# Kernel tuning notes

Measured on AMD Instinct MI355X. Metric: run time of the kernel, lower is better.

## Reference

```python
import jax, jax.numpy as jnp
import numpy as np

BS, H, S, D = 2, 16, 4096, 64
BLOCK = 64
STRIDE_C = 3
NEG = -10000.0


def _global_index(seq_len, block_size, stride_c):
    # static Longformer-style global pattern: first token of each block plus
    # the last `stride_c` tokens of each block
    r = np.arange(seq_len)
    rem = r % block_size
    return np.nonzero((rem == 0) | (rem >= block_size - stride_c))[0]


def setup_inputs() -> dict:
    key = jax.random.key(0)
    k1, k2, k3 = jax.random.split(key, 3)
    q = jax.random.normal(k1, (BS, H, S, D), dtype=jnp.float32)
    k = jax.random.normal(k2, (BS, H, S, D), dtype=jnp.float32)
    v = jax.random.normal(k3, (BS, H, S, D), dtype=jnp.float32)
    mask = jnp.ones((BS, S), dtype=jnp.float32)  # all tokens valid -> pattern is static
    return {"query": q, "key": k, "value": v, "mask": mask}


def reference(query, key, value, mask):
    bs, h, S, d = query.shape
    block = BLOCK
    nb = S // block  # seq_len chosen as multiple of block_size, so pad_len == 0
    g_idx = jnp.asarray(_global_index(S, block, STRIDE_C))  # [G]

    # ---- block-local attention scores ----
    bq = query.reshape(bs, h, nb, block, d)
    bk = key.reshape(bs, h, nb, block, d)
    local = jnp.einsum('bhnxd,bhnyd->bhnxy', bq, bk)  # [bs,h,nb,block,block]
    # additive key-side mask (per key position within each block)
    key_mask = jnp.where(mask == 0.0, NEG, 0.0).reshape(bs, 1, nb, 1, block)
    local = (local + key_mask).reshape(bs, h, S, block)

    # ---- global-token attention scores ----
    gk = key[:, :, g_idx, :]    # [bs,h,G,d]
    gv = value[:, :, g_idx, :]  # [bs,h,G,d]
    gscores = jnp.einsum('bhsd,bhgd->bhsg', query, gk)  # [bs,h,S,G]
    gmask = jnp.where(mask[:, g_idx] == 0.0, NEG, 0.0)[:, None, None, :]
    gscores = gscores + gmask

    # ---- joint softmax over [local block | global tokens] ----
    scores = jnp.concatenate([local, gscores], axis=-1)  # [bs,h,S,block+G]
    probs = jax.nn.softmax(scores.astype(jnp.float32), axis=-1)

    # ---- weighted sums ----
    lp = probs[..., :block].reshape(bs, h, nb, block, block)
    bv = value.reshape(bs, h, nb, block, d)
    lout = jnp.matmul(lp, bv).reshape(bs, h, S, d)
    gout = jnp.einsum('bhsg,bhgd->bhsd', probs[..., block:], gv)
    return lout + gout
```

## Files before the change

### kernel.cpp

```cpp
#include <hip/hip_runtime.h>
#include <math.h>

#define BSZ 2
#define NH 16
#define SEQ 4096
#define DH 64
#define BLK 64
#define NB (SEQ / BLK)
#define NG 256
#define NKEY (BLK + NG)
#define NEGV -10000.0f
#define KSTR 72
#define PSTR2 168

typedef _Float16 f16x8 __attribute__((ext_vector_type(8)));
typedef _Float16 f16x4 __attribute__((ext_vector_type(4)));
typedef float floatx4 __attribute__((ext_vector_type(4)));

__device__ __forceinline__ int gather_row(int g) {
    int j = g >> 2;
    int p = g & 3;
    return j * BLK + (p ? (BLK - 4 + p) : 0);
}

__global__ __launch_bounds__(256, 2)
void sparse_attn_kernel(const float* __restrict__ Q, const float* __restrict__ K,
                        const float* __restrict__ V, const float* __restrict__ M,
                        float* __restrict__ O)
{
    const int wg   = blockIdx.x;
    const int nblk = wg & (NB - 1);
    const int bh   = wg >> 6;
    const int b    = bh >> 4;

    const size_t hoff = (size_t)bh * SEQ * DH;
    const float* Qh = Q + hoff;
    const float* Kh = K + hoff;
    const float* Vh = V + hoff;
    float*       Oh = O + hoff;
    const float* Mb = M + (size_t)b * SEQ;

    __shared__ _Float16 Ksh[NKEY * KSTR];
    __shared__ float    MaskAdd[NKEY];
    _Float16* Psh = Ksh;
    _Float16* VTc = Ksh + 64 * PSTR2;

    const int tid  = threadIdx.x;
    const int lane = tid & 63;
    const int wv   = tid >> 6;
    const int m    = lane & 15;
    const int quad = lane >> 4;

    for (int i = tid; i < NKEY * 16; i += 256) {
        int row = i >> 4;
        int c4  = (i & 15) << 2;
        int srow = (row < BLK) ? (nblk * BLK + row) : gather_row(row - BLK);
        const float4 f = *(const float4*)(Kh + (size_t)srow * DH + c4);
        f16x4 o4;
        o4[0] = (_Float16)f.x; o4[1] = (_Float16)f.y;
        o4[2] = (_Float16)f.z; o4[3] = (_Float16)f.w;
        *(f16x4*)(&Ksh[row * KSTR + c4]) = o4;
    }
    for (int i = tid; i < NKEY; i += 256) {
        int srow = (i < BLK) ? (nblk * BLK + i) : gather_row(i - BLK);
        MaskAdd[i] = (Mb[srow] == 0.0f) ? NEGV : 0.0f;
    }

    const int qrow = nblk * BLK + wv * 16 + m;
    f16x8 qhf[2], qlf[2];
    #pragma unroll
    for (int c = 0; c < 2; ++c) {
        const float* src = Qh + (size_t)qrow * DH + c * 32 + quad * 8;
        float4 f0 = *(const float4*)(src);
        float4 f1 = *(const float4*)(src + 4);
        float vals[8] = {f0.x, f0.y, f0.z, f0.w, f1.x, f1.y, f1.z, f1.w};
        #pragma unroll
        for (int j = 0; j < 8; ++j) {
            _Float16 hi = (_Float16)vals[j];
            float    lo = vals[j] - (float)hi;
            qhf[c][j] = hi;
            qlf[c][j] = (_Float16)lo;
        }
    }

    __syncthreads();

    floatx4 acc[20] = {};
    #pragma unroll
    for (int t = 0; t < 20; ++t) {
        #pragma unroll
        for (int c = 0; c < 2; ++c) {
            f16x8 kf = *(const f16x8*)(&Ksh[(t * 16 + m) * KSTR + c * 32 + quad * 8]);
            acc[t] = __builtin_amdgcn_mfma_f32_16x16x32_f16(qhf[c], kf, acc[t], 0, 0, 0);
            acc[t] = __builtin_amdgcn_mfma_f32_16x16x32_f16(qlf[c], kf, acc[t], 0, 0, 0);
        }
    }

    float rmax[4] = {-3e38f, -3e38f, -3e38f, -3e38f};
    #pragma unroll
    for (int t = 0; t < 20; ++t) {
        float ma = MaskAdd[t * 16 + m];
        #pragma unroll
        for (int r = 0; r < 4; ++r) {
            acc[t][r] += ma;
            rmax[r] = fmaxf(rmax[r], acc[t][r]);
        }
    }
    #pragma unroll
    for (int off = 8; off >= 1; off >>= 1) {
        #pragma unroll
        for (int r = 0; r < 4; ++r)
            rmax[r] = fmaxf(rmax[r], __shfl_xor(rmax[r], off, 64));
    }
    float rsum[4] = {0.f, 0.f, 0.f, 0.f};
    #pragma unroll
    for (int t = 0; t < 20; ++t) {
        #pragma unroll
        for (int r = 0; r < 4; ++r) {
            float e = __expf(acc[t][r] - rmax[r]);
            acc[t][r] = e;
            rsum[r] += e;
        }
    }
    #pragma unroll
    for (int off = 8; off >= 1; off >>= 1) {
        #pragma unroll
        for (int r = 0; r < 4; ++r)
            rsum[r] += __shfl_xor(rsum[r], off, 64);
    }
    float rinv[4];
    #pragma unroll
    for (int r = 0; r < 4; ++r) rinv[r] = 1.0f / rsum[r];

    __syncthreads();

    floatx4 oacc[4] = {};
    for (int cch = 0; cch < 2; ++cch) {
        #pragma unroll
        for (int t = 0; t < 10; ++t) {
            int tt = cch * 10 + t;
            #pragma unroll
            for (int r = 0; r < 4; ++r)
                Psh[(wv * 16 + quad * 4 + r) * PSTR2 + t * 16 + m] =
                    (_Float16)(acc[tt][r] * rinv[r]);
        }
        for (int i = tid; i < 160 * 16; i += 256) {
            int key = (i >> 4) + cch * 160;
            int c4  = (i & 15) << 2;
            int srow = (key < BLK) ? (nblk * BLK + key) : gather_row(key - BLK);
            const float4 f = *(const float4*)(Vh + (size_t)srow * DH + c4);
            int kl = key - cch * 160;
            VTc[(c4 + 0) * PSTR2 + kl] = (_Float16)f.x;
            VTc[(c4 + 1) * PSTR2 + kl] = (_Float16)f.y;
            VTc[(c4 + 2) * PSTR2 + kl] = (_Float16)f.z;
            VTc[(c4 + 3) * PSTR2 + kl] = (_Float16)f.w;
        }
        __syncthreads();
        #pragma unroll
        for (int kc = 0; kc < 5; ++kc) {
            f16x8 pf = *(const f16x8*)(&Psh[(wv * 16 + m) * PSTR2 + kc * 32 + quad * 8]);
            #pragma unroll
            for (int t = 0; t < 4; ++t) {
                f16x8 vf = *(const f16x8*)(&VTc[(t * 16 + m) * PSTR2 + kc * 32 + quad * 8]);
                oacc[t] = __builtin_amdgcn_mfma_f32_16x16x32_f16(pf, vf, oacc[t], 0, 0, 0);
            }
        }
        __syncthreads();
    }

    #pragma unroll
    for (int t = 0; t < 4; ++t) {
        #pragma unroll
        for (int r = 0; r < 4; ++r)
            Oh[(size_t)(nblk * BLK + wv * 16 + quad * 4 + r) * DH + t * 16 + m] = oacc[t][r];
    }
}

extern "C" void kernel_launch(void* const* d_in, const int* in_sizes, int n_in,
                              void* d_out, int out_size, void* d_ws, size_t ws_size,
                              hipStream_t stream) {
    const float* q    = (const float*)d_in[0];
    const float* k    = (const float*)d_in[1];
    const float* v    = (const float*)d_in[2];
    const float* mask = (const float*)d_in[3];
    float* out = (float*)d_out;
    (void)in_sizes; (void)n_in; (void)out_size; (void)d_ws; (void)ws_size;
    sparse_attn_kernel<<<BSZ * NH * NB, 256, 0, stream>>>(q, k, v, mask, out);
}
```

Measured before the change: 181.3 us.

## Rewrite sparse attention kernel with MFMA-native smem layouts and prefetched V

Drops the hi/lo split of Q, so the QK^T MFMA count is halved and precision is lower. K, P and V^T are now stored in shared memory in fragment-contiguous slabs so each lane reads one f16x8 at lane*8. V loads are issued early into registers so they overlap the QK and softmax phases. The mask is folded into the accumulator init and normalization is deferred to the output store. The change also remaps the block index to interleave heads, cuts LDS to raise occupancy to 4 workgroups per CU, and accepts higher register pressure from the prefetched V.

```diff
diff --git a/kernel.cpp b/kernel.cpp
--- a/kernel.cpp
+++ b/kernel.cpp
@@ -1,179 +1,232 @@
 #include <hip/hip_runtime.h>
-#include <math.h>
-
-#define BSZ 2
-#define NH 16
-#define SEQ 4096
-#define DH 64
-#define BLK 64
-#define NB (SEQ / BLK)
-#define NG 256
-#define NKEY (BLK + NG)
+
 #define NEGV -10000.0f
-#define KSTR 72
-#define PSTR2 168
 
 typedef _Float16 f16x8 __attribute__((ext_vector_type(8)));
-typedef _Float16 f16x4 __attribute__((ext_vector_type(4)));
+typedef _Float16 f16x2 __attribute__((ext_vector_type(2)));
 typedef float floatx4 __attribute__((ext_vector_type(4)));
 
-__device__ __forceinline__ int gather_row(int g) {
-    int j = g >> 2;
+__device__ __forceinline__ int src_row(int key, int nblk) {
+    if (key < 64) return nblk * 64 + key;
+    int g = key - 64;
     int p = g & 3;
-    return j * BLK + (p ? (BLK - 4 + p) : 0);
+    return (g >> 2) * 64 + (p ? (60 + p) : 0);
 }
 
-__global__ __launch_bounds__(256, 2)
+__global__ __launch_bounds__(256, 4)
 void sparse_attn_kernel(const float* __restrict__ Q, const float* __restrict__ K,
                         const float* __restrict__ V, const float* __restrict__ M,
                         float* __restrict__ O)
 {
-    const int wg   = blockIdx.x;
-    const int nblk = wg & (NB - 1);
-    const int bh   = wg >> 6;
+    const int x    = blockIdx.x;
+    const int bh   = (x & 7) * 4 + ((x >> 3) >> 6);
+    const int nblk = (x >> 3) & 63;
     const int b    = bh >> 4;
 
-    const size_t hoff = (size_t)bh * SEQ * DH;
+    const size_t hoff = (size_t)bh * (4096 * 64);
     const float* Qh = Q + hoff;
     const float* Kh = K + hoff;
     const float* Vh = V + hoff;
     float*       Oh = O + hoff;
-    const float* Mb = M + (size_t)b * SEQ;
-
-    __shared__ _Float16 Ksh[NKEY * KSTR];
-    __shared__ float    MaskAdd[NKEY];
-    _Float16* Psh = Ksh;
-    _Float16* VTc = Ksh + 64 * PSTR2;
+    const float* Mb = M + (size_t)b * 4096;
+
+    __shared__ _Float16 smem[20480];
+    _Float16* Pbase  = smem;
+    _Float16* VTbase = smem + 10240;
 
     const int tid  = threadIdx.x;
     const int lane = tid & 63;
     const int wv   = tid >> 6;
     const int m    = lane & 15;
     const int quad = lane >> 4;
-
-    for (int i = tid; i < NKEY * 16; i += 256) {
-        int row = i >> 4;
-        int c4  = (i & 15) << 2;
-        int srow = (row < BLK) ? (nblk * BLK + row) : gather_row(row - BLK);
-        const float4 f = *(const float4*)(Kh + (size_t)srow * DH + c4);
-        f16x4 o4;
-        o4[0] = (_Float16)f.x; o4[1] = (_Float16)f.y;
-        o4[2] = (_Float16)f.z; o4[3] = (_Float16)f.w;
-        *(f16x4*)(&Ksh[row * KSTR + c4]) = o4;
-    }
-    for (int i = tid; i < NKEY; i += 256) {
-        int srow = (i < BLK) ? (nblk * BLK + i) : gather_row(i - BLK);
-        MaskAdd[i] = (Mb[srow] == 0.0f) ? NEGV : 0.0f;
-    }
-
-    const int qrow = nblk * BLK + wv * 16 + m;
-    f16x8 qhf[2], qlf[2];
+    const int cg   = tid & 15;
+    const int psub = tid >> 4;
+
+    float mreg[20];
+    #pragma unroll
+    for (int t = 0; t < 20; ++t) {
+        int key = t * 16 + m;
+        mreg[t] = (Mb[src_row(key, nblk)] == 0.0f) ? NEGV : 0.0f;
+    }
+
+    const int qrow = nblk * 64 + wv * 16 + m;
+    f16x8 qf[2];
     #pragma unroll
     for (int c = 0; c < 2; ++c) {
-        const float* src = Qh + (size_t)qrow * DH + c * 32 + quad * 8;
-        float4 f0 = *(const float4*)(src);
+        const float* src = Qh + (size_t)qrow * 64 + c * 32 + quad * 8;
+        float4 f0 = *(const float4*)src;
         float4 f1 = *(const float4*)(src + 4);
-        float vals[8] = {f0.x, f0.y, f0.z, f0.w, f1.x, f1.y, f1.z, f1.w};
-        #pragma unroll
-        for (int j = 0; j < 8; ++j) {
-            _Float16 hi = (_Float16)vals[j];
-            float    lo = vals[j] - (float)hi;
-            qhf[c][j] = hi;
-            qlf[c][j] = (_Float16)lo;
-        }
-    }
-
-    __syncthreads();
-
-    floatx4 acc[20] = {};
+        qf[c][0] = (_Float16)f0.x; qf[c][1] = (_Float16)f0.y;
+        qf[c][2] = (_Float16)f0.z; qf[c][3] = (_Float16)f0.w;
+        qf[c][4] = (_Float16)f1.x; qf[c][5] = (_Float16)f1.y;
+        qf[c][6] = (_Float16)f1.z; qf[c][7] = (_Float16)f1.w;
+    }
+
+    #pragma unroll
+    for (int it = 0; it < 10; ++it) {
+        int S    = it * 256 + tid;
+        int row  = ((S >> 7) * 16) + (S & 15);
+        int col0 = ((S >> 6) & 1) * 32 + ((S & 63) >> 4) * 8;
+        const float* src = Kh + (size_t)src_row(row, nblk) * 64 + col0;
+        float4 f0 = *(const float4*)src;
+        float4 f1 = *(const float4*)(src + 4);
+        f16x8 o;
+        o[0] = (_Float16)f0.x; o[1] = (_Float16)f0.y;
+        o[2] = (_Float16)f0.z; o[3] = (_Float16)f0.w;
+        o[4] = (_Float16)f1.x; o[5] = (_Float16)f1.y;
+        o[6] = (_Float16)f1.z; o[7] = (_Float16)f1.w;
+        *(f16x8*)(&smem[S * 8]) = o;
+    }
+
+    f16x2 vpk[20];
+    #pragma unroll
+    for (int s = 0; s < 5; ++s) {
+        int p = s * 16 + psub;
+        const float4 f0 = *(const float4*)(Vh + (size_t)src_row(2 * p, nblk) * 64 + cg * 4);
+        const float4 f1 = *(const float4*)(Vh + (size_t)src_row(2 * p + 1, nblk) * 64 + cg * 4);
+        vpk[s*4+0][0] = (_Float16)f0.x; vpk[s*4+0][1] = (_Float16)f1.x;
+        vpk[s*4+1][0] = (_Float16)f0.y; vpk[s*4+1][1] = (_Float16)f1.y;
+        vpk[s*4+2][0] = (_Float16)f0.z; vpk[s*4+2][1] = (_Float16)f1.z;
+        vpk[s*4+3][0] = (_Float16)f0.w; vpk[s*4+3][1] = (_Float16)f1.w;
+    }
+
+    __syncthreads();
+
+    floatx4 acc[20];
     #pragma unroll
     for (int t = 0; t < 20; ++t) {
+        float ma = mreg[t];
+        acc[t][0] = ma; acc[t][1] = ma; acc[t][2] = ma; acc[t][3] = ma;
+    }
+    #pragma unroll
+    for (int t = 0; t < 20; ++t) {
         #pragma unroll
         for (int c = 0; c < 2; ++c) {
-            f16x8 kf = *(const f16x8*)(&Ksh[(t * 16 + m) * KSTR + c * 32 + quad * 8]);
-            acc[t] = __builtin_amdgcn_mfma_f32_16x16x32_f16(qhf[c], kf, acc[t], 0, 0, 0);
-            acc[t] = __builtin_amdgcn_mfma_f32_16x16x32_f16(qlf[c], kf, acc[t], 0, 0, 0);
+            f16x8 kf = *(const f16x8*)(&smem[(t * 2 + c) * 512 + lane * 8]);
+            acc[t] = __builtin_amdgcn_mfma_f32_16x16x32_f16(qf[c], kf, acc[t], 0, 0, 0);
         }
     }
 
     float rmax[4] = {-3e38f, -3e38f, -3e38f, -3e38f};
     #pragma unroll
-    for (int t = 0; t < 20; ++t) {
-        float ma = MaskAdd[t * 16 + m];
-        #pragma unroll
-        for (int r = 0; r < 4; ++r) {
-            acc[t][r] += ma;
+    for (int t = 0; t < 20; ++t)
+        #pragma unroll
+        for (int r = 0; r < 4; ++r)
             rmax[r] = fmaxf(rmax[r], acc[t][r]);
-        }
-    }
-    #pragma unroll
-    for (int off = 8; off >= 1; off >>= 1) {
+    #pragma unroll
+    for (int off = 8; off >= 1; off >>= 1)
         #pragma unroll
         for (int r = 0; r < 4; ++r)
             rmax[r] = fmaxf(rmax[r], __shfl_xor(rmax[r], off, 64));
-    }
     float rsum[4] = {0.f, 0.f, 0.f, 0.f};
     #pragma unroll
-    for (int t = 0; t < 20; ++t) {
+    for (int t = 0; t < 20; ++t)
         #pragma unroll
         for (int r = 0; r < 4; ++r) {
             float e = __expf(acc[t][r] - rmax[r]);
             acc[t][r] = e;
             rsum[r] += e;
         }
-    }
-    #pragma unroll
-    for (int off = 8; off >= 1; off >>= 1) {
+    #pragma unroll
+    for (int off = 8; off >= 1; off >>= 1)
         #pragma unroll
         for (int r = 0; r < 4; ++r)
             rsum[r] += __shfl_xor(rsum[r], off, 64);
-    }
     float rinv[4];
     #pragma unroll
     for (int r = 0; r < 4; ++r) rinv[r] = 1.0f / rsum[r];
 
     __syncthreads();
 
+    #pragma unroll
+    for (int tp = 0; tp < 10; ++tp) {
+        int slab = wv * 5 + (tp >> 1);
+        int qa   = (tp & 1) * 2 + (m >> 3);
+        int jj   = m & 7;
+        #pragma unroll
+        for (int r = 0; r < 4; ++r)
+            Pbase[slab * 512 + (qa * 16 + quad * 4 + r) * 8 + jj] = (_Float16)acc[tp][r];
+    }
+    #pragma unroll
+    for (int s = 0; s < 5; ++s) {
+        int rl  = 2 * (s * 16 + psub);
+        int kcl = rl >> 5, qv = (rl & 31) >> 3, jj0 = rl & 7;
+        #pragma unroll
+        for (int e = 0; e < 4; ++e) {
+            int col = cg * 4 + e;
+            *(f16x2*)(&VTbase[((col >> 4) * 5 + kcl) * 512 + (qv * 16 + (col & 15)) * 8 + jj0]) =
+                vpk[s * 4 + e];
+        }
+    }
+    float4 vr0[5], vr1[5];
+    #pragma unroll
+    for (int s = 0; s < 5; ++s) {
+        int p = (5 + s) * 16 + psub;
+        vr0[s] = *(const float4*)(Vh + (size_t)src_row(2 * p, nblk) * 64 + cg * 4);
+        vr1[s] = *(const float4*)(Vh + (size_t)src_row(2 * p + 1, nblk) * 64 + cg * 4);
+    }
+
+    __syncthreads();
+
     floatx4 oacc[4] = {};
-    for (int cch = 0; cch < 2; ++cch) {
-        #pragma unroll
-        for (int t = 0; t < 10; ++t) {
-            int tt = cch * 10 + t;
-            #pragma unroll
-            for (int r = 0; r < 4; ++r)
-                Psh[(wv * 16 + quad * 4 + r) * PSTR2 + t * 16 + m] =
-                    (_Float16)(acc[tt][r] * rinv[r]);
-        }
-        for (int i = tid; i < 160 * 16; i += 256) {
-            int key = (i >> 4) + cch * 160;
-            int c4  = (i & 15) << 2;
-            int srow = (key < BLK) ? (nblk * BLK + key) : gather_row(key - BLK);
-            const float4 f = *(const float4*)(Vh + (size_t)srow * DH + c4);
-            int kl = key - cch * 160;
-            VTc[(c4 + 0) * PSTR2 + kl] = (_Float16)f.x;
-            VTc[(c4 + 1) * PSTR2 + kl] = (_Float16)f.y;
-            VTc[(c4 + 2) * PSTR2 + kl] = (_Float16)f.z;
-            VTc[(c4 + 3) * PSTR2 + kl] = (_Float16)f.w;
-        }
-        __syncthreads();
-        #pragma unroll
-        for (int kc = 0; kc < 5; ++kc) {
-            f16x8 pf = *(const f16x8*)(&Psh[(wv * 16 + m) * PSTR2 + kc * 32 + quad * 8]);
-            #pragma unroll
-            for (int t = 0; t < 4; ++t) {
-                f16x8 vf = *(const f16x8*)(&VTc[(t * 16 + m) * PSTR2 + kc * 32 + quad * 8]);
-                oacc[t] = __builtin_amdgcn_mfma_f32_16x16x32_f16(pf, vf, oacc[t], 0, 0, 0);
-            }
-        }
-        __syncthreads();
-    }
-
-    #pragma unroll
-    for (int t = 0; t < 4; ++t) {
-        #pragma unroll
-        for (int r = 0; r < 4; ++r)
-            Oh[(size_t)(nblk * BLK + wv * 16 + quad * 4 + r) * DH + t * 16 + m] = oacc[t][r];
-    }
+    #pragma unroll
+    for (int kc = 0; kc < 5; ++kc) {
+        f16x8 pf = *(const f16x8*)(&Pbase[(wv * 5 + kc) * 512 + lane * 8]);
+        #pragma unroll
+        for (int t = 0; t < 4; ++t) {
+            f16x8 vf = *(const f16x8*)(&VTbase[(t * 5 + kc) * 512 + lane * 8]);
+            oacc[t] = __builtin_amdgcn_mfma_f32_16x16x32_f16(pf, vf, oacc[t], 0, 0, 0);
+        }
+    }
+
+    __syncthreads();
+
+    #pragma unroll
+    for (int tp = 0; tp < 10; ++tp) {
+        int slab = wv * 5 + (tp >> 1);
+        int qa   = (tp & 1) * 2 + (m >> 3);
+        int jj   = m & 7;
+        #pragma unroll
+        for (int r = 0; r < 4; ++r)
+            Pbase[slab * 512 + (qa * 16 + quad * 4 + r) * 8 + jj] = (_Float16)acc[10 + tp][r];
+    }
+    #pragma unroll
+    for (int s = 0; s < 5; ++s) {
+        int rl  = 2 * ((5 + s) * 16 + psub) - 160;
+        int kcl = rl >> 5, qv = (rl & 31) >> 3, jj0 = rl & 7;
+        const float4 f0 = vr0[s];
+        const float4 f1 = vr1[s];
+        f16x2 pk[4];
+        pk[0][0] = (_Float16)f0.x; pk[0][1] = (_Float16)f1.x;
+        pk[1][0] = (_Float16)f0.y; pk[1][1] = (_Float16)f1.y;
+        pk[2][0] = (_Float16)f0.z; pk[2][1] = (_Float16)f1.z;
+        pk[3][0] = (_Float16)f0.w; pk[3][1] = (_Float16)f1.w;
+        #pragma unroll
+        for (int e = 0; e < 4; ++e) {
+            int col = cg * 4 + e;
+            *(f16x2*)(&VTbase[((col >> 4) * 5 + kcl) * 512 + (qv * 16 + (col & 15)) * 8 + jj0]) =
+                pk[e];
+        }
+    }
+
+    __syncthreads();
+
+    #pragma unroll
+    for (int kc = 0; kc < 5; ++kc) {
+        f16x8 pf = *(const f16x8*)(&Pbase[(wv * 5 + kc) * 512 + lane * 8]);
+        #pragma unroll
+        for (int t = 0; t < 4; ++t) {
+            f16x8 vf = *(const f16x8*)(&VTbase[(t * 5 + kc) * 512 + lane * 8]);
+            oacc[t] = __builtin_amdgcn_mfma_f32_16x16x32_f16(pf, vf, oacc[t], 0, 0, 0);
+        }
+    }
+
+    #pragma unroll
+    for (int t = 0; t < 4; ++t)
+        #pragma unroll
+        for (int r = 0; r < 4; ++r)
+            Oh[(size_t)(nblk * 64 + wv * 16 + quad * 4 + r) * 64 + t * 16 + m] =
+                oacc[t][r] * rinv[r];
 }
 
 extern "C" void kernel_launch(void* const* d_in, const int* in_sizes, int n_in,
@@ -185,5 +238,5 @@
     const float* mask = (const float*)d_in[3];
     float* out = (float*)d_out;
     (void)in_sizes; (void)n_in; (void)out_size; (void)d_ws; (void)ws_size;
-    sparse_attn_kernel<<<BSZ * NH * NB, 256, 0, stream>>>(q, k, v, mask, out);
+    sparse_attn_kernel<<<2 * 16 * 64, 256, 0, stream>>>(q, k, v, mask, out);
 }
```

Result: slower. 187.7 us (+3.5%).
